# Kernel optimization log

Hardware: AMD Instinct MI355X
Metric: run time of the kernel (lower is better)

Reference implementation:

```python
import jax, jax.numpy as jnp
import numpy as np

V, E, S, B, N = 100000, 300, 1024, 64, 5
H = [512, 256, 128]

def setup_inputs() -> dict:
    key = jax.random.key(0)
    ks = jax.random.split(key, 10)
    x = jax.random.randint(ks[0], (B, S), 0, V, dtype=jnp.int32)
    # lengths must be >= n for valid n-gram counts (original assumes this)
    lengths = jax.random.randint(ks[1], (B,), N, S + 1, dtype=jnp.int32)
    sc = lambda f: 1.0 / np.sqrt(f)
    table = jax.random.normal(ks[2], (V, E), dtype=jnp.float32)
    W_slide = jax.random.uniform(ks[3], (N * E, H[0]), jnp.float32, -sc(N * E), sc(N * E))
    b_slide = jax.random.uniform(ks[4], (H[0],), jnp.float32, -sc(N * E), sc(N * E))
    W1 = jax.random.uniform(ks[5], (H[0], H[1]), jnp.float32, -sc(H[0]), sc(H[0]))
    b1 = jax.random.uniform(ks[6], (H[1],), jnp.float32, -sc(H[0]), sc(H[0]))
    W2 = jax.random.uniform(ks[7], (H[1], H[2]), jnp.float32, -sc(H[1]), sc(H[1]))
    b2 = jax.random.uniform(ks[8], (H[2],), jnp.float32, -sc(H[1]), sc(H[1]))
    return {"x": x, "lengths": lengths, "table": table, "W_slide": W_slide,
            "b_slide": b_slide, "W1": W1, "b1": b1, "W2": W2, "b2": b2}

def reference(x, lengths, table, W_slide, b_slide, W1, b1, W2, b2):
    n = N
    Wn = S - (n - 1)  # number of sliding windows per sequence
    emb = table[x]  # [B, S, E]
    # gather sliding windows: [B, Wn, n, E] -> [B, Wn, n*E]
    idx = jnp.arange(Wn)[:, None] + jnp.arange(n)[None, :]
    win = emb[:, idx].reshape(B, Wn, n * E)
    h = win @ W_slide + b_slide              # [B, Wn, H0]
    h = jax.nn.relu(h @ W1 + b1)             # [B, Wn, H1]
    h = jax.nn.relu(h @ W2 + b2)             # [B, Wn, H2]
    # ragged mean over valid n-gram positions per sample
    valid = (lengths - (n - 1)).astype(h.dtype)           # [B]
    mask = (jnp.arange(Wn)[None, :] < (lengths - (n - 1))[:, None]).astype(h.dtype)
    pooled = jnp.einsum('bwh,bw->bh', h, mask) / valid[:, None]
    return pooled
```

## Files before the change

### kernel.cpp

```cpp
#include <hip/hip_runtime.h>

#define B_N    64
#define S_LEN  1024
#define EMB    300
#define EMB_P  304
#define NGRAM  5
#define WPAD   1024
#define MTOT   (B_N * WPAD)
#define K1P    1536
#define H0     512
#define H1D    256
#define H2D    128
#define NK1    (K1P / 32)
#define NSTEP1 (K1P / 64)

#define GATHER_BLOCKS ((MTOT * 38) / 256)
#define WPREP_THREADS (H0 * K1P + H1D * H0 + H2D * H1D)
#define WPREP_BLOCKS  ((WPREP_THREADS + 255) / 256)

typedef _Float16 half8 __attribute__((ext_vector_type(8)));
typedef float  floatx4 __attribute__((ext_vector_type(4)));

typedef const __attribute__((address_space(1))) void* gptr_t;
typedef __attribute__((address_space(3))) void* sptr_t;

__device__ __forceinline__ void gload16(const void* g, void* s) {
  __builtin_amdgcn_global_load_lds((gptr_t)g, (sptr_t)s, 16, 0, 0);
}

__global__ void prep_kernel(const int* __restrict__ x,
                            const int* __restrict__ lengths,
                            const float* __restrict__ table,
                            _Float16* __restrict__ emb,
                            float* __restrict__ out,
                            const float* __restrict__ Ws,
                            const float* __restrict__ W1,
                            const float* __restrict__ W2,
                            _Float16* __restrict__ Bf1,
                            _Float16* __restrict__ Bf2,
                            _Float16* __restrict__ Bf3,
                            int* __restrict__ meta) {
  __shared__ int sN[64], sP[65];
  const int bid = blockIdx.x;
  if (bid < GATHER_BLOCKS) {
    if (bid < 32) out[bid * 256 + threadIdx.x] = 0.0f;
    int tid = bid * 256 + threadIdx.x;
    int tok = tid / 38;
    int c   = tid - tok * 38;
    int valid = lengths[tok >> 10] - (NGRAM - 1);
    int limit = ((valid + 127) & ~127) + (NGRAM - 1);
    if ((tok & 1023) >= limit) return;
    int e = c << 3;
    const float* row = table + (size_t)x[tok] * EMB + e;
    float4 v0 = *(const float4*)row;
    float4 v1 = make_float4(0.0f, 0.0f, 0.0f, 0.0f);
    if (e + 4 < EMB) v1 = *(const float4*)(row + 4);
    union { half8 h8; _Float16 h[8]; } u;
    u.h[0] = (_Float16)v0.x; u.h[1] = (_Float16)v0.y;
    u.h[2] = (_Float16)v0.z; u.h[3] = (_Float16)v0.w;
    u.h[4] = (_Float16)v1.x; u.h[5] = (_Float16)v1.y;
    u.h[6] = (_Float16)v1.z; u.h[7] = (_Float16)v1.w;
    *(half8*)(emb + (size_t)tok * EMB_P + e) = u.h8;
  } else if (bid < GATHER_BLOCKS + WPREP_BLOCKS) {
    int tid = (bid - GATHER_BLOCKS) * 256 + threadIdx.x;
    const int NS = H0 * K1P;
    const int N1 = H1D * H0;
    const int N2 = H2D * H1D;
    if (tid < NS) {
      int n = tid & 511, k = tid >> 9;
      float v = 0.0f;
      if (k < NGRAM * EMB_P) {
        int tn = k / EMB_P, e = k - tn * EMB_P;
        if (e < EMB) v = Ws[(size_t)(tn * EMB + e) * H0 + n];
      }
      int idx = ((((n >> 4) * NK1 + (k >> 5)) << 6) + (((k >> 3) & 3) << 4) + (n & 15)) * 8 + (k & 7);
      Bf1[idx] = (_Float16)v;
    } else if (tid < NS + N1) {
      int t = tid - NS;
      int n = t & 255, k = t >> 8;
      float v = W1[(size_t)k * H1D + n];
      int idx = ((((n >> 4) * 16 + (k >> 5)) << 6) + (((k >> 3) & 3) << 4) + (n & 15)) * 8 + (k & 7);
      Bf2[idx] = (_Float16)v;
    } else if (tid < NS + N1 + N2) {
      int t = tid - (NS + N1);
      int n = t & 127, k = t >> 7;
      float v = W2[(size_t)k * H2D + n];
      int idx = ((((n >> 4) * 8 + (k >> 5)) << 6) + (((k >> 3) & 3) << 4) + (n & 15)) * 8 + (k & 7);
      Bf3[idx] = (_Float16)v;
    }
  } else {
    int t = threadIdx.x;
    if (t < 64) sN[t] = (lengths[t] - (NGRAM - 1) + 127) >> 7;
    __syncthreads();
    if (t == 0) {
      int s = 0;
      for (int i = 0; i < 64; i++) { sP[i] = s; s += sN[i]; }
      sP[64] = s;
      meta[0] = s;
    }
    __syncthreads();
    if (t < 64) {
      int base = sP[t], n = sN[t];
      for (int i = 0; i < n; i++) meta[8 + base + i] = (t << 3) + i;
    }
  }
}

__global__ __launch_bounds__(256, 3)
void gemm1(const _Float16* __restrict__ A, const _Float16* __restrict__ Bf,
           const float* __restrict__ bias, _Float16* __restrict__ Cf,
           const int* __restrict__ meta) {
  __shared__ _Float16 sA[2][128 * 64];

  const int nLive4 = meta[0] << 2;
  const int xcd = blockIdx.x & 7, bi = blockIdx.x >> 3;
  const int q = nLive4 >> 3, r = nLive4 & 7;
  if (bi >= q + (xcd < r ? 1 : 0)) return;
  const int L = xcd * q + (xcd < r ? xcd : r) + bi;
  const int mt = meta[8 + (L >> 2)], nt = L & 3;

  const int tid  = threadIdx.x;
  const int wave = tid >> 6, lane = tid & 63;
  const int wr   = wave >> 1, wc = wave & 1;
  const int quad = lane >> 4, l16 = lane & 15;

  const long mBase = (long)mt << 7;
  const int  nBase = nt << 7;

  const int srow0  = (wave << 3) + (lane >> 3);
  const int schunk = lane & 7;
  const _Float16* aG[4];
  int sOff[4];
#pragma unroll
  for (int p = 0; p < 4; p++) {
    int row = (p << 5) + srow0;
    int c   = schunk ^ (row & 7);
    aG[p]   = A + (mBase + row) * EMB_P + (c << 3);
    sOff[p] = (row << 6) + (schunk << 3);
  }

  const _Float16* bG[4];
#pragma unroll
  for (int j = 0; j < 4; j++)
    bG[j] = Bf + (((size_t)((nBase >> 4) + (wc << 2) + j) * NK1) << 9) + (lane << 3);

  int aOff[2][4];
#pragma unroll
  for (int s = 0; s < 2; s++)
#pragma unroll
    for (int i = 0; i < 4; i++) {
      int rr   = (wr << 6) + (i << 4) + l16;
      int slot = ((s << 2) + quad) ^ (l16 & 7);
      aOff[s][i] = (rr << 6) + (slot << 3);
    }

  floatx4 acc[4][4] = {};

#pragma unroll
  for (int p = 0; p < 4; p++) gload16(aG[p], &sA[0][sOff[p]]);
  half8 bCur[2][4], bNxt[2][4];
#pragma unroll
  for (int s = 0; s < 2; s++)
#pragma unroll
    for (int j = 0; j < 4; j++)
      bCur[s][j] = *(const half8*)(bG[j] + ((size_t)s << 9));

#pragma unroll 2
  for (int kk = 0; kk < NSTEP1; kk++) {
    const int cur = kk & 1;
    __syncthreads();
    if (kk + 1 < NSTEP1) {
      const int ko = (kk + 1) << 6;
#pragma unroll
      for (int p = 0; p < 4; p++) gload16(aG[p] + ko, &sA[cur ^ 1][sOff[p]]);
#pragma unroll
      for (int s = 0; s < 2; s++)
#pragma unroll
        for (int j = 0; j < 4; j++)
          bNxt[s][j] = *(const half8*)(bG[j] + (size_t)((((kk + 1) << 1) + s) << 9));
    }
#pragma unroll
    for (int s = 0; s < 2; s++) {
      half8 aFr[4];
#pragma unroll
      for (int i = 0; i < 4; i++)
        aFr[i] = *(const half8*)(&sA[cur][aOff[s][i]]);
#pragma unroll
      for (int i = 0; i < 4; i++)
#pragma unroll
        for (int j = 0; j < 4; j++)
          acc[i][j] = __builtin_amdgcn_mfma_f32_16x16x32_f16(aFr[i], bCur[s][j], acc[i][j], 0, 0, 0);
    }
#pragma unroll
    for (int s = 0; s < 2; s++)
#pragma unroll
      for (int j = 0; j < 4; j++)
        bCur[s][j] = bNxt[s][j];
  }

  __syncthreads();
  _Float16* cs = &sA[0][0];
#pragma unroll
  for (int j = 0; j < 4; j++) {
    int cl = (wc << 6) + (j << 4) + l16;
    float bv = bias[nBase + cl];
    int ksl = cl >> 5;
    int sub_hi = ((cl >> 3) & 3) << 4;
    int c7 = cl & 7;
#pragma unroll
    for (int i = 0; i < 4; i++) {
      int m16l = (wr << 2) + i;
#pragma unroll
      for (int rr = 0; rr < 4; rr++) {
        int ml = (quad << 2) + rr;
        cs[(((m16l << 2) + ksl) << 9) + ((sub_hi + ml) << 3) + c7] =
            (_Float16)(acc[i][j][rr] + bv);
      }
    }
  }
  __syncthreads();
#pragma unroll
  for (int it = 0; it < 8; it++) {
    int cid = (it << 2) + wave;
    int m16l = cid >> 2, ksl = cid & 3;
    size_t g = ((size_t)(((mt << 3) + m16l) * 16 + (nt << 2) + ksl) << 9) + (lane << 3);
    *(half8*)(Cf + g) = *(const half8*)(cs + (cid << 9) + (lane << 3));
  }
}

__global__ __launch_bounds__(256, 2)
void gemm23(const _Float16* __restrict__ Af, const _Float16* __restrict__ B2,
            const _Float16* __restrict__ B3, const float* __restrict__ bias1,
            const float* __restrict__ bias2, float* __restrict__ out,
            const int* __restrict__ lengths, const int* __restrict__ meta) {
  __shared__ _Float16 sH[32768];
  __shared__ float red[2][128];

  if ((int)blockIdx.x >= meta[0]) return;
  const int mt = meta[8 + blockIdx.x];

  const int tid  = threadIdx.x;
  const int wave = tid >> 6, lane = tid & 63;
  const int wr   = wave >> 1, wc = wave & 1;
  const int quad = lane >> 4, l16 = lane & 15;

  const int b = mt >> 3;
  const int validw = lengths[b] - (NGRAM - 1);

  const _Float16* aB = Af + (((size_t)((mt << 3) + (wr << 2)) * 16) << 9) + (lane << 3);
  const _Float16* bB = B2 + ((size_t)wc << 16) + (lane << 3);

  floatx4 acc2[4][8] = {};
  half8 aP[4], bP[8], aQ[4], bQ[8];

  auto loadA = [&](half8* d, int kk) {
#pragma unroll
    for (int i = 0; i < 4; i++)
      d[i] = *(const half8*)(aB + ((size_t)kk << 9) + ((size_t)i << 13));
  };
  auto loadB = [&](half8* d, int kk) {
#pragma unroll
    for (int j = 0; j < 8; j++)
      d[j] = *(const half8*)(bB + ((size_t)kk << 9) + ((size_t)j << 13));
  };
  auto mfmaStep = [&](const half8* aF, const half8* bF) {
#pragma unroll
    for (int i = 0; i < 4; i++)
#pragma unroll
      for (int j = 0; j < 8; j++)
        acc2[i][j] = __builtin_amdgcn_mfma_f32_16x16x32_f16(aF[i], bF[j], acc2[i][j], 0, 0, 0);
  };

  loadA(aP, 0); loadB(bP, 0);
#pragma unroll
  for (int kk = 0; kk < 16; kk += 2) {
    loadA(aQ, kk + 1); loadB(bQ, kk + 1);
    mfmaStep(aP, bP);
    if (kk + 2 < 16) { loadA(aP, kk + 2); loadB(bP, kk + 2); }
    mfmaStep(aQ, bQ);
  }

#pragma unroll
  for (int j = 0; j < 8; j++) {
    int n = (wc << 7) + (j << 4) + l16;
    float bv = bias1[n];
    int ks = n >> 5;
    int sub_hi = ((n >> 3) & 3) << 4;
    int c7 = n & 7;
#pragma unroll
    for (int i = 0; i < 4; i++) {
      int m16l = (wr << 2) + i;
#pragma unroll
      for (int rr = 0; rr < 4; rr++) {
        int ml = (quad << 2) + rr;
        sH[(((m16l << 3) + ks) << 9) + ((sub_hi + ml) << 3) + c7] =
            (_Float16)fmaxf(acc2[i][j][rr] + bv, 0.0f);
      }
    }
  }
  __syncthreads();

  const _Float16* b3R[4];
#pragma unroll
  for (int j = 0; j < 4; j++)
    b3R[j] = B3 + (((size_t)((wc << 2) + j) * 8) << 9) + (lane << 3);

  floatx4 acc3[4][4] = {};
#pragma unroll
  for (int ks = 0; ks < 8; ks++) {
    half8 aF[4], bF[4];
#pragma unroll
    for (int i = 0; i < 4; i++)
      aF[i] = *(const half8*)(sH + (((((wr << 2) + i) << 3) + ks) << 9) + (lane << 3));
#pragma unroll
    for (int j = 0; j < 4; j++) bF[j] = *(const half8*)(b3R[j] + ((size_t)ks << 9));
#pragma unroll
    for (int i = 0; i < 4; i++)
#pragma unroll
      for (int j = 0; j < 4; j++)
        acc3[i][j] = __builtin_amdgcn_mfma_f32_16x16x32_f16(aF[i], bF[j], acc3[i][j], 0, 0, 0);
  }

  float inv = 1.0f / (float)validw;
  int wBase = ((mt & 7) << 7) + (wr << 6);
#pragma unroll
  for (int j = 0; j < 4; j++) {
    int col = (wc << 6) + (j << 4) + l16;
    float bv = bias2[col];
    float p = 0.0f;
#pragma unroll
    for (int i = 0; i < 4; i++) {
#pragma unroll
      for (int rr = 0; rr < 4; rr++) {
        int w = wBase + (i << 4) + (quad << 2) + rr;
        float v = fmaxf(acc3[i][j][rr] + bv, 0.0f);
        p += (w < validw) ? v : 0.0f;
      }
    }
    p *= inv;
    p += __shfl_xor(p, 16, 64);
    p += __shfl_xor(p, 32, 64);
    if (quad == 0) red[wr][col] = p;
  }
  __syncthreads();
  if (tid < 128) atomicAdd(out + b * H2D + tid, red[0][tid] + red[1][tid]);
}

extern "C" void kernel_launch(void* const* d_in, const int* in_sizes, int n_in,
                              void* d_out, int out_size, void* d_ws, size_t ws_size,
                              hipStream_t stream) {
  const int*   x       = (const int*)d_in[0];
  const int*   lengths = (const int*)d_in[1];
  const float* table   = (const float*)d_in[2];
  const float* W_slide = (const float*)d_in[3];
  const float* b_slide = (const float*)d_in[4];
  const float* W1      = (const float*)d_in[5];
  const float* b1      = (const float*)d_in[6];
  const float* W2      = (const float*)d_in[7];
  const float* b2      = (const float*)d_in[8];
  float* out = (float*)d_out;

  _Float16* ws  = (_Float16*)d_ws;
  _Float16* emb = ws;
  _Float16* Bf1 = emb + (size_t)MTOT * EMB_P + 4096;
  _Float16* Bf2 = Bf1 + (size_t)H0 * K1P;
  _Float16* Bf3 = Bf2 + (size_t)H1D * H0;
  _Float16* h1f = Bf3 + (size_t)H2D * H1D;
  int*      meta = (int*)(h1f + (size_t)MTOT * H0);

  prep_kernel<<<GATHER_BLOCKS + WPREP_BLOCKS + 1, 256, 0, stream>>>(
      x, lengths, table, emb, out, W_slide, W1, W2, Bf1, Bf2, Bf3, meta);
  gemm1<<<(MTOT / 128) * (H0 / 128), 256, 0, stream>>>(emb, Bf1, b_slide, h1f, meta);
  gemm23<<<MTOT / 128, 256, 0, stream>>>(h1f, Bf2, Bf3, b1, b2, out, lengths, meta);
}
```

Baseline: 276.3 us.

## Shrink gemm23 row tile to 64, split prep kernel, add MFMA priority

The fused layer-2/3 kernel now handles 64-row tiles instead of 128, with each of the four waves owning a column slice. A second per-sample tile list with 64-row granularity is built in metadata, so padding work for ragged lengths is reduced and more blocks run (occupancy bound raised to 3). The LDS reduction is replaced by direct per-wave atomics, and s_setprio is wrapped around the MFMA loops. The prep kernel is split into separate gather and weight-prep launches, which adds one launch but removes branch divergence. In exchange, every 64-row tile reloads the W1/W2 weights and more atomics are issued.

```diff
diff --git a/kernel.cpp b/kernel.cpp
--- a/kernel.cpp
+++ b/kernel.cpp
@@ -28,41 +28,44 @@
   __builtin_amdgcn_global_load_lds((gptr_t)g, (sptr_t)s, 16, 0, 0);
 }
 
-__global__ void prep_kernel(const int* __restrict__ x,
-                            const int* __restrict__ lengths,
-                            const float* __restrict__ table,
-                            _Float16* __restrict__ emb,
-                            float* __restrict__ out,
-                            const float* __restrict__ Ws,
-                            const float* __restrict__ W1,
-                            const float* __restrict__ W2,
-                            _Float16* __restrict__ Bf1,
-                            _Float16* __restrict__ Bf2,
-                            _Float16* __restrict__ Bf3,
-                            int* __restrict__ meta) {
-  __shared__ int sN[64], sP[65];
+__global__ void gatherk(const int* __restrict__ x,
+                        const int* __restrict__ lengths,
+                        const float* __restrict__ table,
+                        _Float16* __restrict__ emb,
+                        float* __restrict__ out) {
   const int bid = blockIdx.x;
-  if (bid < GATHER_BLOCKS) {
-    if (bid < 32) out[bid * 256 + threadIdx.x] = 0.0f;
+  if (bid < 32) out[bid * 256 + threadIdx.x] = 0.0f;
+  int tid = bid * 256 + threadIdx.x;
+  int tok = tid / 38;
+  int c   = tid - tok * 38;
+  int valid = lengths[tok >> 10] - (NGRAM - 1);
+  int limit = ((valid + 127) & ~127) + (NGRAM - 1);
+  if ((tok & 1023) >= limit) return;
+  int e = c << 3;
+  const float* row = table + (size_t)x[tok] * EMB + e;
+  float4 v0 = *(const float4*)row;
+  float4 v1 = make_float4(0.0f, 0.0f, 0.0f, 0.0f);
+  if (e + 4 < EMB) v1 = *(const float4*)(row + 4);
+  union { half8 h8; _Float16 h[8]; } u;
+  u.h[0] = (_Float16)v0.x; u.h[1] = (_Float16)v0.y;
+  u.h[2] = (_Float16)v0.z; u.h[3] = (_Float16)v0.w;
+  u.h[4] = (_Float16)v1.x; u.h[5] = (_Float16)v1.y;
+  u.h[6] = (_Float16)v1.z; u.h[7] = (_Float16)v1.w;
+  *(half8*)(emb + (size_t)tok * EMB_P + e) = u.h8;
+}
+
+__global__ void wprepk(const int* __restrict__ lengths,
+                       const float* __restrict__ Ws,
+                       const float* __restrict__ W1,
+                       const float* __restrict__ W2,
+                       _Float16* __restrict__ Bf1,
+                       _Float16* __restrict__ Bf2,
+                       _Float16* __restrict__ Bf3,
+                       int* __restrict__ meta) {
+  __shared__ int sN[64], sP[65], sN6[64], sP6[65];
+  const int bid = blockIdx.x;
+  if (bid < WPREP_BLOCKS) {
     int tid = bid * 256 + threadIdx.x;
-    int tok = tid / 38;
-    int c   = tid - tok * 38;
-    int valid = lengths[tok >> 10] - (NGRAM - 1);
-    int limit = ((valid + 127) & ~127) + (NGRAM - 1);
-    if ((tok & 1023) >= limit) return;
-    int e = c << 3;
-    const float* row = table + (size_t)x[tok] * EMB + e;
-    float4 v0 = *(const float4*)row;
-    float4 v1 = make_float4(0.0f, 0.0f, 0.0f, 0.0f);
-    if (e + 4 < EMB) v1 = *(const float4*)(row + 4);
-    union { half8 h8; _Float16 h[8]; } u;
-    u.h[0] = (_Float16)v0.x; u.h[1] = (_Float16)v0.y;
-    u.h[2] = (_Float16)v0.z; u.h[3] = (_Float16)v0.w;
-    u.h[4] = (_Float16)v1.x; u.h[5] = (_Float16)v1.y;
-    u.h[6] = (_Float16)v1.z; u.h[7] = (_Float16)v1.w;
-    *(half8*)(emb + (size_t)tok * EMB_P + e) = u.h8;
-  } else if (bid < GATHER_BLOCKS + WPREP_BLOCKS) {
-    int tid = (bid - GATHER_BLOCKS) * 256 + threadIdx.x;
     const int NS = H0 * K1P;
     const int N1 = H1D * H0;
     const int N2 = H2D * H1D;
@@ -90,18 +93,26 @@
     }
   } else {
     int t = threadIdx.x;
-    if (t < 64) sN[t] = (lengths[t] - (NGRAM - 1) + 127) >> 7;
+    if (t < 64) {
+      int valid = lengths[t] - (NGRAM - 1);
+      sN[t]  = (valid + 127) >> 7;
+      sN6[t] = (valid + 63) >> 6;
+    }
     __syncthreads();
     if (t == 0) {
-      int s = 0;
-      for (int i = 0; i < 64; i++) { sP[i] = s; s += sN[i]; }
-      sP[64] = s;
-      meta[0] = s;
+      int s = 0, s6 = 0;
+      for (int i = 0; i < 64; i++) {
+        sP[i] = s;  s  += sN[i];
+        sP6[i] = s6; s6 += sN6[i];
+      }
+      meta[0] = s; meta[1] = s6;
     }
     __syncthreads();
     if (t < 64) {
       int base = sP[t], n = sN[t];
       for (int i = 0; i < n; i++) meta[8 + base + i] = (t << 3) + i;
+      int b6 = sP6[t], n6 = sN6[t];
+      for (int i = 0; i < n6; i++) meta[520 + b6 + i] = (t << 4) + i;
     }
   }
 }
@@ -228,30 +239,29 @@
   }
 }
 
-__global__ __launch_bounds__(256, 2)
+__global__ __launch_bounds__(256, 3)
 void gemm23(const _Float16* __restrict__ Af, const _Float16* __restrict__ B2,
             const _Float16* __restrict__ B3, const float* __restrict__ bias1,
             const float* __restrict__ bias2, float* __restrict__ out,
             const int* __restrict__ lengths, const int* __restrict__ meta) {
-  __shared__ _Float16 sH[32768];
-  __shared__ float red[2][128];
-
-  if ((int)blockIdx.x >= meta[0]) return;
-  const int mt = meta[8 + blockIdx.x];
+  __shared__ _Float16 sH[16384];
+
+  if ((int)blockIdx.x >= meta[1]) return;
+  const int mt = meta[520 + blockIdx.x];
 
   const int tid  = threadIdx.x;
   const int wave = tid >> 6, lane = tid & 63;
-  const int wr   = wave >> 1, wc = wave & 1;
+  const int wc   = wave;
   const int quad = lane >> 4, l16 = lane & 15;
 
-  const int b = mt >> 3;
+  const int b = mt >> 4;
   const int validw = lengths[b] - (NGRAM - 1);
 
-  const _Float16* aB = Af + (((size_t)((mt << 3) + (wr << 2)) * 16) << 9) + (lane << 3);
-  const _Float16* bB = B2 + ((size_t)wc << 16) + (lane << 3);
-
-  floatx4 acc2[4][8] = {};
-  half8 aP[4], bP[8], aQ[4], bQ[8];
+  const _Float16* aB = Af + (((size_t)(mt << 2) * 16) << 9) + (lane << 3);
+  const _Float16* bB = B2 + ((size_t)wc << 15) + (lane << 3);
+
+  floatx4 acc2[4][4] = {};
+  half8 aP[4], bP[4], aQ[4], bQ[4];
 
   auto loadA = [&](half8* d, int kk) {
 #pragma unroll
@@ -260,15 +270,17 @@
   };
   auto loadB = [&](half8* d, int kk) {
 #pragma unroll
-    for (int j = 0; j < 8; j++)
+    for (int j = 0; j < 4; j++)
       d[j] = *(const half8*)(bB + ((size_t)kk << 9) + ((size_t)j << 13));
   };
   auto mfmaStep = [&](const half8* aF, const half8* bF) {
+    __builtin_amdgcn_s_setprio(1);
 #pragma unroll
     for (int i = 0; i < 4; i++)
 #pragma unroll
-      for (int j = 0; j < 8; j++)
+      for (int j = 0; j < 4; j++)
         acc2[i][j] = __builtin_amdgcn_mfma_f32_16x16x32_f16(aF[i], bF[j], acc2[i][j], 0, 0, 0);
+    __builtin_amdgcn_s_setprio(0);
   };
 
   loadA(aP, 0); loadB(bP, 0);
@@ -281,51 +293,52 @@
   }
 
 #pragma unroll
-  for (int j = 0; j < 8; j++) {
-    int n = (wc << 7) + (j << 4) + l16;
+  for (int j = 0; j < 4; j++) {
+    int n = (wc << 6) + (j << 4) + l16;
     float bv = bias1[n];
     int ks = n >> 5;
     int sub_hi = ((n >> 3) & 3) << 4;
     int c7 = n & 7;
 #pragma unroll
     for (int i = 0; i < 4; i++) {
-      int m16l = (wr << 2) + i;
 #pragma unroll
       for (int rr = 0; rr < 4; rr++) {
         int ml = (quad << 2) + rr;
-        sH[(((m16l << 3) + ks) << 9) + ((sub_hi + ml) << 3) + c7] =
+        sH[(((i << 3) + ks) << 9) + ((sub_hi + ml) << 3) + c7] =
             (_Float16)fmaxf(acc2[i][j][rr] + bv, 0.0f);
       }
     }
   }
   __syncthreads();
 
-  const _Float16* b3R[4];
-#pragma unroll
-  for (int j = 0; j < 4; j++)
-    b3R[j] = B3 + (((size_t)((wc << 2) + j) * 8) << 9) + (lane << 3);
-
-  floatx4 acc3[4][4] = {};
+  const _Float16* b3R[2];
+#pragma unroll
+  for (int j = 0; j < 2; j++)
+    b3R[j] = B3 + (((size_t)((wc << 1) + j) * 8) << 9) + (lane << 3);
+
+  floatx4 acc3[4][2] = {};
 #pragma unroll
   for (int ks = 0; ks < 8; ks++) {
-    half8 aF[4], bF[4];
+    half8 aF[4], bF[2];
 #pragma unroll
     for (int i = 0; i < 4; i++)
-      aF[i] = *(const half8*)(sH + (((((wr << 2) + i) << 3) + ks) << 9) + (lane << 3));
-#pragma unroll
-    for (int j = 0; j < 4; j++) bF[j] = *(const half8*)(b3R[j] + ((size_t)ks << 9));
+      aF[i] = *(const half8*)(sH + (((i << 3) + ks) << 9) + (lane << 3));
+#pragma unroll
+    for (int j = 0; j < 2; j++) bF[j] = *(const half8*)(b3R[j] + ((size_t)ks << 9));
+    __builtin_amdgcn_s_setprio(1);
 #pragma unroll
     for (int i = 0; i < 4; i++)
 #pragma unroll
-      for (int j = 0; j < 4; j++)
+      for (int j = 0; j < 2; j++)
         acc3[i][j] = __builtin_amdgcn_mfma_f32_16x16x32_f16(aF[i], bF[j], acc3[i][j], 0, 0, 0);
+    __builtin_amdgcn_s_setprio(0);
   }
 
   float inv = 1.0f / (float)validw;
-  int wBase = ((mt & 7) << 7) + (wr << 6);
-#pragma unroll
-  for (int j = 0; j < 4; j++) {
-    int col = (wc << 6) + (j << 4) + l16;
+  int wBase = (mt & 15) << 6;
+#pragma unroll
+  for (int j = 0; j < 2; j++) {
+    int col = (wc << 5) + (j << 4) + l16;
     float bv = bias2[col];
     float p = 0.0f;
 #pragma unroll
@@ -340,10 +353,8 @@
     p *= inv;
     p += __shfl_xor(p, 16, 64);
     p += __shfl_xor(p, 32, 64);
-    if (quad == 0) red[wr][col] = p;
-  }
-  __syncthreads();
-  if (tid < 128) atomicAdd(out + b * H2D + tid, red[0][tid] + red[1][tid]);
+    if (quad == 0) atomicAdd(out + b * H2D + col, p);
+  }
 }
 
 extern "C" void kernel_launch(void* const* d_in, const int* in_sizes, int n_in,
@@ -368,8 +379,9 @@
   _Float16* h1f = Bf3 + (size_t)H2D * H1D;
   int*      meta = (int*)(h1f + (size_t)MTOT * H0);
 
-  prep_kernel<<<GATHER_BLOCKS + WPREP_BLOCKS + 1, 256, 0, stream>>>(
-      x, lengths, table, emb, out, W_slide, W1, W2, Bf1, Bf2, Bf3, meta);
+  gatherk<<<GATHER_BLOCKS, 256, 0, stream>>>(x, lengths, table, emb, out);
+  wprepk<<<WPREP_BLOCKS + 1, 256, 0, stream>>>(lengths, W_slide, W1, W2,
+                                               Bf1, Bf2, Bf3, meta);
   gemm1<<<(MTOT / 128) * (H0 / 128), 256, 0, stream>>>(emb, Bf1, b_slide, h1f, meta);
-  gemm23<<<MTOT / 128, 256, 0, stream>>>(h1f, Bf2, Bf3, b1, b2, out, lengths, meta);
-}
+  gemm23<<<MTOT / 64, 256, 0, stream>>>(h1f, Bf2, Bf3, b1, b2, out, lengths, meta);
+}
```

Result: no change. 272.5 us (-1.4%).
